# Kernel tuning notes

Hardware: AMD Instinct MI355X
Metric: run time of the kernel (lower is better)

Reference implementation:

```python
import jax, jax.numpy as jnp
import numpy as np

N, E, D = 524288, 50000, 64
COMMITMENT_COST = 0.25
EPS = 1e-6


def setup_inputs() -> dict:
    key = jax.random.key(0)
    k1, k2, k3 = jax.random.split(key, 3)
    inputs_all = jax.random.normal(k1, (N, D + 1), dtype=jnp.float32)
    # sorted unique genus taxids (even integers) -> codebook rows 0..E-1
    genus_taxids_key = (2 * jnp.arange(E)).astype(jnp.int32)
    taxids = jax.random.randint(k2, (N,), 0, 2 * E, dtype=jnp.int32)
    lineages_all = jnp.stack([jnp.full((N,), -1, jnp.int32), taxids], axis=1)
    # original inits embeddings to zeros; use small noise so the manifold map is non-degenerate
    embeddings = 0.01 * jax.random.normal(k3, (E, D), dtype=jnp.float32)
    return {"inputs_all": inputs_all, "lineages_all": lineages_all,
            "embeddings": embeddings, "genus_taxids_key": genus_taxids_key}


def convert_codebook_lorentz(w):
    # w: [*, D] -> hyperboloid points [*, D+1]
    x = 3.0 * jnp.tanh(w)
    # Lorentz_inner_product(v, v) with v = pad(x, (1,0)) is sum(x^2)
    n = jnp.sqrt(jnp.clip(jnp.sum(x * x, axis=-1, keepdims=True), EPS, None))
    n = jnp.clip(n, None, 10.0)
    v = jnp.concatenate([jnp.zeros_like(n), x], axis=-1)          # [*, D+1]
    mu0 = jnp.concatenate([jnp.ones_like(n), jnp.zeros_like(x)], axis=-1)
    return jnp.cosh(n) * mu0 + jnp.sinh(n) * v / n


def geodesic_distance(a, b):
    lip = jnp.sum(a[..., 1:] * b[..., 1:], axis=-1) - a[..., 0] * b[..., 0]
    return jnp.arccosh(jnp.clip(-lip, 1.0 + EPS, None))


def reference(inputs_all, lineages_all, embeddings, genus_taxids_key):
    taxids = lineages_all[:, 1]
    # GPU-resident replacement of the host dict lookup: keys are sorted
    idx = jnp.searchsorted(genus_taxids_key, taxids)
    idx = jnp.clip(idx, 0, genus_taxids_key.shape[0] - 1)
    mask = genus_taxids_key[idx] == taxids                        # [N] bool, torch.isin

    quantized = convert_codebook_lorentz(embeddings[idx])         # [N, D+1]
    e_latent = geodesic_distance(jax.lax.stop_gradient(quantized), inputs_all)
    q_latent = geodesic_distance(quantized, jax.lax.stop_gradient(inputs_all))
    c_loss = q_latent + COMMITMENT_COST * e_latent                # [N]

    n_valid = jnp.maximum(jnp.sum(mask.astype(jnp.float32)), 1.0)
    mean_loss = jnp.sum(jnp.where(mask, c_loss, 0.0)) / n_valid   # mean over valid rows

    quantized_st = inputs_all + jax.lax.stop_gradient(quantized - inputs_all)
    quantized_all = jnp.where(mask[:, None], quantized_st, inputs_all)
    return mean_loss, quantized_all
```

## Files before the change

kernel.cpp:

```cpp
#include <hip/hip_runtime.h>


#define NBLOCKS 2048
#define NTHREADS 256
#define WAVES_PER_BLOCK (NTHREADS / 64)

__device__ __forceinline__ float waveReduceSum(float v) {
#pragma unroll
    for (int m = 32; m >= 1; m >>= 1) v += __shfl_xor(v, m, 64);
    return v;
}

__device__ __forceinline__ float fast_tanh(float x) {
    x = fminf(fmaxf(x, -15.0f), 15.0f);
    float e2 = __expf(2.0f * x);
    return (e2 - 1.0f) * __builtin_amdgcn_rcpf(e2 + 1.0f);
}

__global__ __launch_bounds__(256) void vq_table_init(int* __restrict__ table, int ts) {
    int i = blockIdx.x * 256 + threadIdx.x;
    if (i < ts) table[i] = -1;
}

__global__ __launch_bounds__(256) void vq_table_fill(const int* __restrict__ key,
                                                     int* __restrict__ table,
                                                     int E, int ts) {
    int i = blockIdx.x * 256 + threadIdx.x;
    if (i < E) {
        int k = key[i];
        if ((unsigned)k < (unsigned)ts) table[k] = i;
    }
}

__global__ __launch_bounds__(256) void vq_codebook(const float* __restrict__ emb,
                                                   float* __restrict__ cb, int E) {
    const int lane = threadIdx.x & 63;
    const int wave = (blockIdx.x * NTHREADS + threadIdx.x) >> 6;
    if (wave >= E) return;
    const float w = emb[(size_t)wave * 64 + lane];
    const float x = 3.0f * fast_tanh(w);
    float n2 = waveReduceSum(x * x);
    n2 = fmaxf(n2, 1e-6f);
    float n = fminf(sqrtf(n2), 10.0f);
    const float e  = __expf(n);
    const float ei = __builtin_amdgcn_rcpf(e);
    const float c  = 0.5f * (e + ei);
    const float s  = 0.5f * (e - ei) * __builtin_amdgcn_rcpf(n);
    float* cbRow = cb + (size_t)wave * 65;
    cbRow[1 + lane] = s * x;
    if (lane == 0) cbRow[0] = c;
}

struct RowCtx {
    const float* inputs;
    const int*   lineages;
    const float* cb;
    const int*   table;
    float*       out;
    int          ts;
};

__device__ __forceinline__ void process_row(const RowCtx& c, int row, int lane,
                                            float& lossAcc, float& cntAcc) {
    const int t = c.lineages[2 * (size_t)row + 1];
    const int idx = ((unsigned)t < (unsigned)c.ts) ? c.table[t] : -1;

    const float* inRow = c.inputs + (size_t)row * 65;
    const float in0 = inRow[0];
    const float ind = inRow[1 + lane];
    float* outRow = c.out + 1 + (size_t)row * 65;

    if (idx >= 0) {
        const float* cbRow = c.cb + (size_t)idx * 65;
        const float cc = cbRow[0];
        const float qd = cbRow[1 + lane];
        const float dot = waveReduceSum(qd * ind);
        const float lip = dot - cc * in0;
        const float z = fmaxf(-lip, 1.0f + 1e-6f);
        const float dist = __logf(z + sqrtf(fmaxf(z * z - 1.0f, 0.0f)));
        if (lane == 0) { lossAcc += 1.25f * dist; cntAcc += 1.0f; }
        outRow[1 + lane] = qd;
        if (lane == 0) outRow[0] = cc;
    } else {
        outRow[1 + lane] = ind;
        if (lane == 0) outRow[0] = in0;
    }
}

__global__ __launch_bounds__(NTHREADS) void vq_main(
    const float* __restrict__ inputs,
    const int*   __restrict__ lineages,
    const float* __restrict__ cb,
    const int*   __restrict__ table,
    float* __restrict__ out,
    float* __restrict__ partialLoss,
    float* __restrict__ partialCnt,
    int N, int ts)
{
    const int lane        = threadIdx.x & 63;
    const int waveInBlock = threadIdx.x >> 6;
    const int waveGlobal  = blockIdx.x * WAVES_PER_BLOCK + waveInBlock;
    const int totalWaves  = gridDim.x * WAVES_PER_BLOCK;
    const int half        = N >> 1;

    RowCtx c{inputs, lineages, cb, table, out, ts};
    float lossAcc = 0.0f, cntAcc = 0.0f;

    for (int row = waveGlobal; row < half; row += totalWaves) {
        process_row(c, row,        lane, lossAcc, cntAcc);
        process_row(c, row + half, lane, lossAcc, cntAcc);
    }

    __shared__ float sLoss[WAVES_PER_BLOCK];
    __shared__ float sCnt[WAVES_PER_BLOCK];
    if (lane == 0) { sLoss[waveInBlock] = lossAcc; sCnt[waveInBlock] = cntAcc; }
    __syncthreads();
    if (threadIdx.x == 0) {
        float L = 0.0f, C = 0.0f;
#pragma unroll
        for (int i = 0; i < WAVES_PER_BLOCK; i++) { L += sLoss[i]; C += sCnt[i]; }
        partialLoss[blockIdx.x] = L;
        partialCnt[blockIdx.x]  = C;
    }
}

__global__ __launch_bounds__(256) void vq_finalize(
    const float* __restrict__ partialLoss,
    const float* __restrict__ partialCnt,
    float* __restrict__ out, int nParts)
{
    __shared__ float sL[256];
    __shared__ float sC[256];
    float L = 0.0f, C = 0.0f;
    for (int i = threadIdx.x; i < nParts; i += 256) {
        L += partialLoss[i];
        C += partialCnt[i];
    }
    sL[threadIdx.x] = L; sC[threadIdx.x] = C;
    __syncthreads();
    if (threadIdx.x == 0) {
        float tl = 0.0f, tc = 0.0f;
        for (int i = 0; i < 256; i++) { tl += sL[i]; tc += sC[i]; }
        out[0] = tl / fmaxf(tc, 1.0f);
    }
}

extern "C" void kernel_launch(void* const* d_in, const int* in_sizes, int n_in,
                              void* d_out, int out_size, void* d_ws, size_t ws_size,
                              hipStream_t stream) {
    const float* inputs   = (const float*)d_in[0];
    const int*   lineages = (const int*)d_in[1];
    const float* emb      = (const float*)d_in[2];
    const int*   key      = (const int*)d_in[3];
    const int E = in_sizes[3];
    const int N = in_sizes[0] / 65;
    const int ts = 2 * E;

    float* out = (float*)d_out;
    char*  ws  = (char*)d_ws;
    int*   table = (int*)ws;
    float* cb    = (float*)(ws + (size_t)ts * sizeof(int));
    float* partialLoss = cb + (size_t)E * 65;
    float* partialCnt  = partialLoss + NBLOCKS;

    vq_table_init<<<(ts + 255) / 256, 256, 0, stream>>>(table, ts);
    vq_table_fill<<<(E + 255) / 256, 256, 0, stream>>>(key, table, E, ts);
    vq_codebook<<<(E * 64 + NTHREADS - 1) / NTHREADS, NTHREADS, 0, stream>>>(emb, cb, E);
    vq_main<<<NBLOCKS, NTHREADS, 0, stream>>>(inputs, lineages, cb, table,
                                              out, partialLoss, partialCnt, N, ts);
    vq_finalize<<<1, 256, 0, stream>>>(partialLoss, partialCnt, out, NBLOCKS);
}
```

Baseline: 375.3 us.

## Batch per-row lookups into 64-row chunks and broadcast via readlane

```diff
diff --git a/kernel.cpp b/kernel.cpp
--- a/kernel.cpp
+++ b/kernel.cpp
@@ -4,6 +4,7 @@
 #define NBLOCKS 2048
 #define NTHREADS 256
 #define WAVES_PER_BLOCK (NTHREADS / 64)
+#define CHUNK 64
 
 __device__ __forceinline__ float waveReduceSum(float v) {
 #pragma unroll
@@ -51,42 +52,6 @@
     if (lane == 0) cbRow[0] = c;
 }
 
-struct RowCtx {
-    const float* inputs;
-    const int*   lineages;
-    const float* cb;
-    const int*   table;
-    float*       out;
-    int          ts;
-};
-
-__device__ __forceinline__ void process_row(const RowCtx& c, int row, int lane,
-                                            float& lossAcc, float& cntAcc) {
-    const int t = c.lineages[2 * (size_t)row + 1];
-    const int idx = ((unsigned)t < (unsigned)c.ts) ? c.table[t] : -1;
-
-    const float* inRow = c.inputs + (size_t)row * 65;
-    const float in0 = inRow[0];
-    const float ind = inRow[1 + lane];
-    float* outRow = c.out + 1 + (size_t)row * 65;
-
-    if (idx >= 0) {
-        const float* cbRow = c.cb + (size_t)idx * 65;
-        const float cc = cbRow[0];
-        const float qd = cbRow[1 + lane];
-        const float dot = waveReduceSum(qd * ind);
-        const float lip = dot - cc * in0;
-        const float z = fmaxf(-lip, 1.0f + 1e-6f);
-        const float dist = __logf(z + sqrtf(fmaxf(z * z - 1.0f, 0.0f)));
-        if (lane == 0) { lossAcc += 1.25f * dist; cntAcc += 1.0f; }
-        outRow[1 + lane] = qd;
-        if (lane == 0) outRow[0] = cc;
-    } else {
-        outRow[1 + lane] = ind;
-        if (lane == 0) outRow[0] = in0;
-    }
-}
-
 __global__ __launch_bounds__(NTHREADS) void vq_main(
     const float* __restrict__ inputs,
     const int*   __restrict__ lineages,
@@ -101,14 +66,73 @@
     const int waveInBlock = threadIdx.x >> 6;
     const int waveGlobal  = blockIdx.x * WAVES_PER_BLOCK + waveInBlock;
     const int totalWaves  = gridDim.x * WAVES_PER_BLOCK;
-    const int half        = N >> 1;
+    const int nChunks     = (N + CHUNK - 1) / CHUNK;
 
-    RowCtx c{inputs, lineages, cb, table, out, ts};
     float lossAcc = 0.0f, cntAcc = 0.0f;
 
-    for (int row = waveGlobal; row < half; row += totalWaves) {
-        process_row(c, row,        lane, lossAcc, cntAcc);
-        process_row(c, row + half, lane, lossAcc, cntAcc);
+    for (int chunk = waveGlobal; chunk < nChunks; chunk += totalWaves) {
+        const int base = chunk * CHUNK;
+
+        if (base + CHUNK <= N) {
+            const int myRow   = base + lane;
+            const int   t_l   = lineages[2 * (size_t)myRow + 1];
+            const float in0_l = inputs[(size_t)myRow * 65];
+            const int   idx_l = ((unsigned)t_l < (unsigned)ts) ? table[t_l] : -1;
+            float c_l = in0_l;
+
+#pragma unroll 8
+            for (int j = 0; j < CHUNK; ++j) {
+                const int   sidx    = __builtin_amdgcn_readlane(idx_l, j);
+                const float in0     = __uint_as_float(
+                    __builtin_amdgcn_readlane(__float_as_uint(in0_l), j));
+                const bool  matched = sidx >= 0;
+
+                const float* cbRow = cb + (size_t)(matched ? sidx : 0) * 65;
+                const float cc = cbRow[0];
+                const float qd = cbRow[1 + lane];
+                const float* inRow = inputs + (size_t)(base + j) * 65;
+                const float ind = inRow[1 + lane];
+
+                const float dot = waveReduceSum(qd * ind);
+                const float lip = dot - cc * in0;
+                const float z   = fmaxf(-lip, 1.0f + 1e-6f);
+                const float dist = __logf(z + sqrtf(fmaxf(z * z - 1.0f, 0.0f)));
+                lossAcc += matched ? 1.25f * dist : 0.0f;
+                cntAcc  += matched ? 1.0f : 0.0f;
+
+                out[1 + (size_t)(base + j) * 65 + 1 + lane] = matched ? qd : ind;
+                const float tc = matched ? cc : in0;
+                c_l = (lane == j) ? tc : c_l;
+            }
+            out[1 + (size_t)myRow * 65] = c_l;
+        } else {
+            for (int j = 0; j < CHUNK; ++j) {
+                const int row = base + j;
+                if (row >= N) break;
+                const int t = lineages[2 * (size_t)row + 1];
+                const int idx = ((unsigned)t < (unsigned)ts) ? table[t] : -1;
+                const float* inRow = inputs + (size_t)row * 65;
+                const float in0 = inRow[0];
+                const float ind = inRow[1 + lane];
+                float* outRow = out + 1 + (size_t)row * 65;
+                if (idx >= 0) {
+                    const float* cbRow = cb + (size_t)idx * 65;
+                    const float cc = cbRow[0];
+                    const float qd = cbRow[1 + lane];
+                    const float dot = waveReduceSum(qd * ind);
+                    const float z = fmaxf(-(dot - cc * in0), 1.0f + 1e-6f);
+                    const float dist = __logf(z + sqrtf(fmaxf(z * z - 1.0f, 0.0f)));
+                    if (lane == 0) { lossAcc += 1.25f * dist; cntAcc += 1.0f; }
+                    lossAcc = __shfl(lossAcc, 0, 64);
+                    cntAcc  = __shfl(cntAcc, 0, 64);
+                    outRow[1 + lane] = qd;
+                    if (lane == 0) outRow[0] = cc;
+                } else {
+                    outRow[1 + lane] = ind;
+                    if (lane == 0) outRow[0] = in0;
+                }
+            }
+        }
     }
 
     __shared__ float sLoss[WAVES_PER_BLOCK];
```

Result: faster. 319.4 us (-14.9%).
